# Optimization experiments

Measured on AMD Instinct MI355X. Metric: run time of the kernel, lower is better.

The kernel has to match this reference:

```python
import jax, jax.numpy as jnp
import numpy as np

B, C, H, W = 4, 512, 64, 64


def setup_inputs() -> dict:
    key = jax.random.key(0)
    k1, k2, k3, k4, k5 = jax.random.split(key, 5)
    s = 0.02
    return {
        "x": jax.random.normal(k1, (B, C, H, W), dtype=jnp.float32),
        "qkv_w": jax.random.normal(k2, (3 * C, C), dtype=jnp.float32) * s,
        "qkv_b": jax.random.normal(k3, (3 * C,), dtype=jnp.float32) * s,
        "proj_w": jax.random.normal(k4, (C, C), dtype=jnp.float32) * s,
        "proj_b": jax.random.normal(k5, (C,), dtype=jnp.float32) * s,
    }


def reference(x, qkv_w, qkv_b, proj_w, proj_b):
    # NOTE: the original module creates a GroupNorm but never calls it in
    # forward(), so x feeds the 1x1 qkv conv directly.
    b, c, h, w_ = x.shape
    n = h * w_
    xf = x.reshape(b, c, n)  # [B, C, N]
    # 1x1 conv == channel matmul
    qkv = jnp.einsum('oc,bcn->bon', qkv_w, xf) + qkv_b[None, :, None]  # [B, 3C, N]
    q, k, v = qkv[:, :c], qkv[:, c:2 * c], qkv[:, 2 * c:]
    scale = jnp.float32(c) ** -0.5
    # scores[b, i, j] = q_i . k_j  (i, j over spatial positions)
    scores = jnp.einsum('bci,bcj->bij', q, k) * scale  # [B, N, N]
    attn = jax.nn.softmax(scores, axis=2)
    # out_i = sum_j attn[i, j] * v_j
    hmat = jnp.einsum('bij,bcj->bci', attn, v)  # [B, C, N]
    out = jnp.einsum('oc,bcn->bon', proj_w, hmat) + proj_b[None, :, None]
    return x + out.reshape(b, c, h, w_)
```

## Files before the change

### kernel.cpp

```cpp
#include <hip/hip_runtime.h>


using u16 = unsigned short;
using u32 = unsigned int;
using h8   = __attribute__((ext_vector_type(8)))  short;
using fx4  = __attribute__((ext_vector_type(4)))  float;
using q16  = __attribute__((ext_vector_type(4)))  u32;
using u16x4= __attribute__((ext_vector_type(4)))  u16;

#define BB 4
#define CC 512
#define NN 4096
#define NBE ((size_t)BB * NN * CC)

#define GLOBAL_AS __attribute__((address_space(1)))
#define LDS_AS    __attribute__((address_space(3)))
#define GLOAD_LDS(src, dst) \
  __builtin_amdgcn_global_load_lds((const GLOBAL_AS u32*)(const void*)(src), \
                                   (LDS_AS u32*)(void*)(dst), 16, 0, 0)

__device__ __forceinline__ u16 f2b(float f) {
  u32 u = __float_as_uint(f);
  u = (u + 0x7fffu + ((u >> 16) & 1u)) >> 16;
  return (u16)u;
}
__device__ __forceinline__ float b2f(u16 h) { return __uint_as_float(((u32)h) << 16); }

__global__ void k_prep(const float* __restrict__ qw, const float* __restrict__ pw,
                       u16* __restrict__ wqb, u16* __restrict__ wpb) {
  int i = blockIdx.x * 256 + threadIdx.x;
  if (i < 1536 * 512) wqb[i] = f2b(qw[i]);
  if (i < 512 * 512)  wpb[i] = f2b(pw[i]);
}

__global__ __launch_bounds__(256) void k_txp(const float* __restrict__ x, u16* __restrict__ xt) {
  int bid = blockIdx.x;
  int nb = bid & 63; int cb = (bid >> 6) & 7; int b = bid >> 9;
  __shared__ float t[64][65];
  const float* xb = x + (size_t)b * CC * NN;
  for (int k = 0; k < 16; ++k) {
    int idx = k * 256 + threadIdx.x;
    int r = idx >> 6, col = idx & 63;
    t[r][col] = xb[(size_t)(cb * 64 + r) * NN + nb * 64 + col];
  }
  __syncthreads();
  u16* xtb = xt + (size_t)b * NN * CC;
  for (int k = 0; k < 16; ++k) {
    int idx = k * 256 + threadIdx.x;
    int nr = idx >> 6, cc = idx & 63;
    xtb[(size_t)(nb * 64 + nr) * CC + cb * 64 + cc] = f2b(t[cc][nr]);
  }
}

__device__ __forceinline__ void gemm_mm(const char* __restrict__ Ab, const char* __restrict__ Bb,
                                        q16* aT, q16* bT, fx4 (&acc)[4][4], int tid) {
  const int lane = tid & 63, wv = tid >> 6;
  const int wm = wv >> 1, wn = wv & 1, g = lane >> 4, r = lane & 15;
  for (int kb = 0; kb < 8; ++kb) {
    __syncthreads();
#pragma unroll
    for (int it = 0; it < 4; ++it) {
      int idx = it * 256 + tid; int row = idx >> 3, slot = idx & 7;
      size_t go = (size_t)row * 1024 + (size_t)kb * 128 + (size_t)slot * 16;
      aT[row * 8 + (slot ^ (row & 7))] = *(const q16*)(Ab + go);
      bT[row * 8 + (slot ^ (row & 7))] = *(const q16*)(Bb + go);
    }
    __syncthreads();
#pragma unroll
    for (int ks = 0; ks < 2; ++ks) {
      h8 af[4], bf[4];
#pragma unroll
      for (int mt = 0; mt < 4; ++mt) { int row = wm * 64 + mt * 16 + r; af[mt] = *(const h8*)&aT[row * 8 + ((ks * 4 + g) ^ (row & 7))]; }
#pragma unroll
      for (int nt = 0; nt < 4; ++nt) { int row = wn * 64 + nt * 16 + r; bf[nt] = *(const h8*)&bT[row * 8 + ((ks * 4 + g) ^ (row & 7))]; }
#pragma unroll
      for (int mt = 0; mt < 4; ++mt)
#pragma unroll
        for (int nt = 0; nt < 4; ++nt)
          acc[mt][nt] = __builtin_amdgcn_mfma_f32_16x16x32_bf16(af[mt], bf[nt], acc[mt][nt], 0, 0, 0);
    }
  }
}

__global__ __launch_bounds__(256) void k_qkv(const u16* __restrict__ wqb, const u16* __restrict__ xt,
                                             const float* __restrict__ qkvb,
                                             u16* __restrict__ qt, u16* __restrict__ kt, u16* __restrict__ vv) {
  __shared__ q16 aT[1024], bT[1024];
  int bid = blockIdx.x;
  int nb = bid & 31; int mb = (bid >> 5) % 12; int b = bid / 384;
  int ob = mb * 128, n0 = nb * 128;
  int tid = threadIdx.x, lane = tid & 63, wv = tid >> 6;
  int wm = wv >> 1, wn = wv & 1, g = lane >> 4, r = lane & 15;
  fx4 acc[4][4] = {};
  gemm_mm((const char*)(wqb + (size_t)ob * CC),
          (const char*)(xt + ((size_t)b * NN + n0) * CC), aT, bT, acc, tid);
  int region = mb >> 2;
#pragma unroll
  for (int mt = 0; mt < 4; ++mt) {
    int o_b = ob + wm * 64 + mt * 16 + g * 4;
#pragma unroll
    for (int nt = 0; nt < 4; ++nt) {
      int n = n0 + wn * 64 + nt * 16 + r;
      if (region == 2) {
#pragma unroll
        for (int rr = 0; rr < 4; ++rr) {
          int o = o_b + rr;
          float v = acc[mt][nt][rr] + qkvb[o];
          vv[((size_t)b * CC + (o - 1024)) * NN + n] = f2b(v);
        }
      } else {
        u16x4 pk;
#pragma unroll
        for (int rr = 0; rr < 4; ++rr) {
          int o = o_b + rr;
          float v = acc[mt][nt][rr] + qkvb[o];
          if (region == 0) v *= 0.044194173824159216f;
          pk[rr] = f2b(v);
        }
        u16* dst = (region == 0 ? qt : kt) + ((size_t)b * NN + n) * CC + (o_b - region * 512);
        *(u16x4*)dst = pk;
      }
    }
  }
}

#define BAR_VM() do { asm volatile("s_waitcnt vmcnt(0) lgkmcnt(0)" ::: "memory"); \
  __builtin_amdgcn_sched_barrier(0); __builtin_amdgcn_s_barrier(); \
  __builtin_amdgcn_sched_barrier(0); } while (0)

__global__ __launch_bounds__(512, 1) void k_attn(const u16* __restrict__ qt, const u16* __restrict__ kt,
                                                 const u16* __restrict__ vv,
                                                 u16* __restrict__ op, float* __restrict__ ml) {
  __shared__ __align__(16) q16 kbuf[2][2048];
  __shared__ __align__(16) q16 vbuf[2][2048];
  __shared__ __align__(16) u16 pT[8][16][40];

  int bid = blockIdx.x;
  int bp = bid & 7; int b = bp >> 1, part = bp & 1;
  int qb0 = (bid >> 3) * 128;
  int tid = threadIdx.x, w = tid >> 6, l = tid & 63;
  int g = l >> 4, r = l & 15;

  const u16* ktb = kt + (size_t)b * NN * CC;
  const u16* vvb = vv + (size_t)b * CC * NN;
  int j0 = part * 2048;

  h8 qf[16];
  {
    const u16* qrow = qt + ((size_t)b * NN + qb0 + w * 16 + r) * CC + g * 8;
#pragma unroll
    for (int ks = 0; ks < 16; ++ks) qf[ks] = *(const h8*)(qrow + ks * 32);
  }

  h8 ones;
#pragma unroll
  for (int e = 0; e < 8; ++e) ones[e] = (short)0x3F80;

  fx4 oacc[32] = {};
  fx4 lacc = {};

  const u16* ksrc0 = ktb + (size_t)w * CC + (size_t)((l ^ w) * 8);
  const int  vxr   = (l >> 3) & 3;
  const u16* vsrc0 = vvb + (size_t)(w * 16 + (l >> 2)) * NN + ((l & 3) ^ vxr) * 8;

#define STAGE(JB, D) do { \
  _Pragma("unroll") \
  for (int ro = 0; ro < 4; ++ro) { \
    int row = ro * 8 + w; \
    GLOAD_LDS(ksrc0 + ((size_t)(JB) + ro * 8) * CC, &kbuf[D][row * 64]); \
  } \
  _Pragma("unroll") \
  for (int ro = 0; ro < 4; ++ro) { \
    GLOAD_LDS(vsrc0 + (size_t)ro * 128 * NN + (JB), &vbuf[D][ro * 512 + w * 64]); \
  } \
} while (0)

  STAGE(j0, 0);
  BAR_VM();

  int cur = 0;
  for (int t = 0; t < 64; ++t) {
    if (t < 63) STAGE(j0 + t * 32 + 32, cur ^ 1);

    fx4 s[2] = {};
#pragma unroll
    for (int ks = 0; ks < 16; ++ks) {
#pragma unroll
      for (int nt = 0; nt < 2; ++nt) {
        int row = nt * 16 + r;
        h8 kf = *(const h8*)&kbuf[cur][row * 64 + ((ks * 4 + g) ^ (r & 7))];
        s[nt] = __builtin_amdgcn_mfma_f32_16x16x32_bf16(qf[ks], kf, s[nt], 0, 0, 0);
      }
    }

#pragma unroll
    for (int rr = 0; rr < 4; ++rr) {
      pT[w][g * 4 + rr][r]      = f2b(__expf(s[0][rr]));
      pT[w][g * 4 + rr][16 + r] = f2b(__expf(s[1][rr]));
    }
    asm volatile("s_waitcnt lgkmcnt(0)" ::: "memory");
    __builtin_amdgcn_sched_barrier(0);

    h8 pf = *(const h8*)&pT[w][r][g * 8];
    lacc = __builtin_amdgcn_mfma_f32_16x16x32_bf16(pf, ones, lacc, 0, 0, 0);
#pragma unroll
    for (int ct = 0; ct < 32; ++ct) {
      int c = ct * 16 + r;
      h8 vf = *(const h8*)&vbuf[cur][c * 4 + (g ^ ((r >> 1) & 3))];
      oacc[ct] = __builtin_amdgcn_mfma_f32_16x16x32_bf16(pf, vf, oacc[ct], 0, 0, 0);
    }

    BAR_VM();
    cur ^= 1;
  }

  u16* opb = op + (((size_t)part * BB + b) * NN + qb0 + w * 16) * CC;
#pragma unroll
  for (int ct = 0; ct < 32; ++ct)
#pragma unroll
    for (int rr = 0; rr < 4; ++rr) {
      int i = g * 4 + rr; int c = ct * 16 + r;
      opb[(size_t)i * CC + c] = f2b(oacc[ct][rr]);
    }
  if (r == 0) {
#pragma unroll
    for (int rr = 0; rr < 4; ++rr)
      ml[((size_t)part * BB + b) * NN + qb0 + w * 16 + g * 4 + rr] = lacc[rr];
  }
}

__global__ __launch_bounds__(256) void k_proj(const u16* __restrict__ op, const float* __restrict__ ml,
                                              const u16* __restrict__ wpb,
                                              const float* __restrict__ pb, const float* __restrict__ x,
                                              float* __restrict__ out) {
  __shared__ q16 aT[1024], bT[1024];
  __shared__ float invl[128];
  int bid = blockIdx.x;
  int ot = bid & 3; int ntile = (bid >> 2) & 31; int b = bid >> 7;
  int n0 = ntile * 128, o0 = ot * 128;
  int tid = threadIdx.x, lane = tid & 63, wv = tid >> 6;
  int wm = wv >> 1, wn = wv & 1, g = lane >> 4, r = lane & 15;

  if (tid < 128) {
    int n = n0 + tid;
    float l1 = ml[((size_t)0 * BB + b) * NN + n];
    float l2 = ml[((size_t)1 * BB + b) * NN + n];
    invl[tid] = 1.0f / (l1 + l2);
  }

  const char* Ab1 = (const char*)(op + ((size_t)b * NN + n0) * CC);
  const char* Ab2 = Ab1 + NBE * sizeof(u16);
  const char* Bb  = (const char*)(wpb + (size_t)o0 * CC);
  fx4 acc[4][4] = {};
  for (int kb = 0; kb < 8; ++kb) {
    __syncthreads();
#pragma unroll
    for (int it = 0; it < 4; ++it) {
      int idx = it * 256 + tid; int row = idx >> 3, slot = idx & 7;
      size_t go = (size_t)row * 1024 + (size_t)kb * 128 + (size_t)slot * 16;
      q16 a1 = *(const q16*)(Ab1 + go);
      q16 a2 = *(const q16*)(Ab2 + go);
      float iv = invl[row];
      u16 res[8];
      const u16* pa1 = (const u16*)&a1; const u16* pa2 = (const u16*)&a2;
#pragma unroll
      for (int e = 0; e < 8; ++e) res[e] = f2b((b2f(pa1[e]) + b2f(pa2[e])) * iv);
      aT[row * 8 + (slot ^ (row & 7))] = *(const q16*)res;
      bT[row * 8 + (slot ^ (row & 7))] = *(const q16*)(Bb + go);
    }
    __syncthreads();
#pragma unroll
    for (int ks = 0; ks < 2; ++ks) {
      h8 af[4], bf[4];
#pragma unroll
      for (int mt = 0; mt < 4; ++mt) { int row = wm * 64 + mt * 16 + r; af[mt] = *(const h8*)&aT[row * 8 + ((ks * 4 + g) ^ (row & 7))]; }
#pragma unroll
      for (int nt = 0; nt < 4; ++nt) { int row = wn * 64 + nt * 16 + r; bf[nt] = *(const h8*)&bT[row * 8 + ((ks * 4 + g) ^ (row & 7))]; }
#pragma unroll
      for (int mt = 0; mt < 4; ++mt)
#pragma unroll
        for (int nt = 0; nt < 4; ++nt)
          acc[mt][nt] = __builtin_amdgcn_mfma_f32_16x16x32_bf16(af[mt], bf[nt], acc[mt][nt], 0, 0, 0);
    }
  }
  const float* xb = x + (size_t)b * CC * NN;
  float* ob_ = out + (size_t)b * CC * NN;
#pragma unroll
  for (int nt = 0; nt < 4; ++nt) {
    int o = o0 + wn * 64 + nt * 16 + r;
    float bias = pb[o];
#pragma unroll
    for (int mt = 0; mt < 4; ++mt) {
      int n = n0 + wm * 64 + mt * 16 + g * 4;
      fx4 xv = *(const fx4*)(xb + (size_t)o * NN + n);
      fx4 res;
#pragma unroll
      for (int rr = 0; rr < 4; ++rr) res[rr] = acc[mt][nt][rr] + bias + xv[rr];
      *(fx4*)(ob_ + (size_t)o * NN + n) = res;
    }
  }
}

extern "C" void kernel_launch(void* const* d_in, const int* in_sizes, int n_in,
                              void* d_out, int out_size, void* d_ws, size_t ws_size,
                              hipStream_t stream) {
  const float* x  = (const float*)d_in[0];
  const float* qw = (const float*)d_in[1];
  const float* qb = (const float*)d_in[2];
  const float* pw = (const float*)d_in[3];
  const float* pb = (const float*)d_in[4];
  float* out = (float*)d_out;

  u16* ws  = (u16*)d_ws;
  u16* qt  = ws;
  u16* kt  = qt + NBE;
  u16* vv  = kt + NBE;
  u16* xt  = vv + NBE;
  u16* wqb = xt + NBE;
  u16* wpb = wqb + 1536 * 512;
  u16* op  = wpb + 512 * 512;
  float* ml = (float*)(op + 2 * NBE);

  hipLaunchKernelGGL(k_prep, dim3(3072), dim3(256), 0, stream, qw, pw, wqb, wpb);
  hipLaunchKernelGGL(k_txp,  dim3(2048), dim3(256), 0, stream, x, xt);
  hipLaunchKernelGGL(k_qkv,  dim3(1536), dim3(256), 0, stream, wqb, xt, qb, qt, kt, vv);
  hipLaunchKernelGGL(k_attn, dim3(256),  dim3(512), 0, stream, qt, kt, vv, op, ml);
  hipLaunchKernelGGL(k_proj, dim3(512),  dim3(256), 0, stream, op, ml, wpb, pb, x, out);
}
```

Measured before the change: 356.3 us.

## Switch attention Q/K/V and probabilities to FP8 MFMA

```diff
diff --git a/kernel.cpp b/kernel.cpp
--- a/kernel.cpp
+++ b/kernel.cpp
@@ -1,6 +1,7 @@
 #include <hip/hip_runtime.h>
 
 
+using u8  = unsigned char;
 using u16 = unsigned short;
 using u32 = unsigned int;
 using h8   = __attribute__((ext_vector_type(8)))  short;
@@ -12,6 +13,7 @@
 #define CC 512
 #define NN 4096
 #define NBE ((size_t)BB * NN * CC)
+#define SCALE 0.044194173824159216f
 
 #define GLOBAL_AS __attribute__((address_space(1)))
 #define LDS_AS    __attribute__((address_space(3)))
@@ -25,6 +27,9 @@
   return (u16)u;
 }
 __device__ __forceinline__ float b2f(u16 h) { return __uint_as_float(((u32)h) << 16); }
+__device__ __forceinline__ u8 f2f8(float f) {
+  return (u8)(u32)__builtin_amdgcn_cvt_pk_fp8_f32(f, 0.f, 0, false);
+}
 
 __global__ void k_prep(const float* __restrict__ qw, const float* __restrict__ pw,
                        u16* __restrict__ wqb, u16* __restrict__ wpb) {
@@ -84,7 +89,7 @@
 
 __global__ __launch_bounds__(256) void k_qkv(const u16* __restrict__ wqb, const u16* __restrict__ xt,
                                              const float* __restrict__ qkvb,
-                                             u16* __restrict__ qt, u16* __restrict__ kt, u16* __restrict__ vv) {
+                                             u8* __restrict__ qt, u8* __restrict__ kt, u8* __restrict__ vv) {
   __shared__ q16 aT[1024], bT[1024];
   int bid = blockIdx.x;
   int nb = bid & 31; int mb = (bid >> 5) % 12; int b = bid / 384;
@@ -101,24 +106,21 @@
 #pragma unroll
     for (int nt = 0; nt < 4; ++nt) {
       int n = n0 + wn * 64 + nt * 16 + r;
+      float v0 = acc[mt][nt][0] + qkvb[o_b + 0];
+      float v1 = acc[mt][nt][1] + qkvb[o_b + 1];
+      float v2 = acc[mt][nt][2] + qkvb[o_b + 2];
+      float v3 = acc[mt][nt][3] + qkvb[o_b + 3];
       if (region == 2) {
-#pragma unroll
-        for (int rr = 0; rr < 4; ++rr) {
-          int o = o_b + rr;
-          float v = acc[mt][nt][rr] + qkvb[o];
-          vv[((size_t)b * CC + (o - 1024)) * NN + n] = f2b(v);
-        }
+        u8* vb = vv + ((size_t)b * CC + (o_b - 1024)) * NN + n;
+        vb[0]          = f2f8(v0);
+        vb[NN]         = f2f8(v1);
+        vb[2 * NN]     = f2f8(v2);
+        vb[3 * (size_t)NN] = f2f8(v3);
       } else {
-        u16x4 pk;
-#pragma unroll
-        for (int rr = 0; rr < 4; ++rr) {
-          int o = o_b + rr;
-          float v = acc[mt][nt][rr] + qkvb[o];
-          if (region == 0) v *= 0.044194173824159216f;
-          pk[rr] = f2b(v);
-        }
-        u16* dst = (region == 0 ? qt : kt) + ((size_t)b * NN + n) * CC + (o_b - region * 512);
-        *(u16x4*)dst = pk;
+        int t = __builtin_amdgcn_cvt_pk_fp8_f32(v0, v1, 0, false);
+        t = __builtin_amdgcn_cvt_pk_fp8_f32(v2, v3, t, true);
+        u8* dst = (region == 0 ? qt : kt) + ((size_t)b * NN + n) * CC + (o_b - region * 512);
+        *(u32*)dst = (u32)t;
       }
     }
   }
@@ -128,12 +130,12 @@
   __builtin_amdgcn_sched_barrier(0); __builtin_amdgcn_s_barrier(); \
   __builtin_amdgcn_sched_barrier(0); } while (0)
 
-__global__ __launch_bounds__(512, 1) void k_attn(const u16* __restrict__ qt, const u16* __restrict__ kt,
-                                                 const u16* __restrict__ vv,
+__global__ __launch_bounds__(512, 1) void k_attn(const u8* __restrict__ qt, const u8* __restrict__ kt,
+                                                 const u8* __restrict__ vv,
                                                  u16* __restrict__ op, float* __restrict__ ml) {
-  __shared__ __align__(16) q16 kbuf[2][2048];
-  __shared__ __align__(16) q16 vbuf[2][2048];
-  __shared__ __align__(16) u16 pT[8][16][40];
+  __shared__ __align__(16) q16 kbuf[2][1024];
+  __shared__ __align__(16) q16 vbuf[2][1024];
+  __shared__ __align__(16) u8 pT[8][16][40];
 
   int bid = blockIdx.x;
   int bp = bid & 7; int b = bp >> 1, part = bp & 1;
@@ -141,38 +143,35 @@
   int tid = threadIdx.x, w = tid >> 6, l = tid & 63;
   int g = l >> 4, r = l & 15;
 
-  const u16* ktb = kt + (size_t)b * NN * CC;
-  const u16* vvb = vv + (size_t)b * CC * NN;
+  const u8* ktb = kt + (size_t)b * NN * CC;
+  const u8* vvb = vv + (size_t)b * CC * NN;
   int j0 = part * 2048;
 
-  h8 qf[16];
+  long qf[16];
   {
-    const u16* qrow = qt + ((size_t)b * NN + qb0 + w * 16 + r) * CC + g * 8;
-#pragma unroll
-    for (int ks = 0; ks < 16; ++ks) qf[ks] = *(const h8*)(qrow + ks * 32);
-  }
-
-  h8 ones;
-#pragma unroll
-  for (int e = 0; e < 8; ++e) ones[e] = (short)0x3F80;
+    const u8* qrow = qt + ((size_t)b * NN + qb0 + w * 16 + r) * CC + g * 8;
+#pragma unroll
+    for (int ks = 0; ks < 16; ++ks) qf[ks] = *(const long*)(qrow + ks * 32);
+  }
+
+  const long ones8 = 0x3838383838383838L;
 
   fx4 oacc[32] = {};
   fx4 lacc = {};
 
-  const u16* ksrc0 = ktb + (size_t)w * CC + (size_t)((l ^ w) * 8);
-  const int  vxr   = (l >> 3) & 3;
-  const u16* vsrc0 = vvb + (size_t)(w * 16 + (l >> 2)) * NN + ((l & 3) ^ vxr) * 8;
+  const int rk = w * 2 + (l >> 5);
+  const int ck = l & 31;
+  const size_t koff = (size_t)rk * CC + (size_t)((ck ^ (rk & 7)) * 16);
+  const int kdst = rk * 32 + ck;
+  const size_t voff = (size_t)(w * 32 + (l >> 1)) * NN + (l & 1) * 16;
+  const int vdst = (w * 32 + (l >> 1)) * 2 + (l & 1);
 
 #define STAGE(JB, D) do { \
-  _Pragma("unroll") \
-  for (int ro = 0; ro < 4; ++ro) { \
-    int row = ro * 8 + w; \
-    GLOAD_LDS(ksrc0 + ((size_t)(JB) + ro * 8) * CC, &kbuf[D][row * 64]); \
-  } \
-  _Pragma("unroll") \
-  for (int ro = 0; ro < 4; ++ro) { \
-    GLOAD_LDS(vsrc0 + (size_t)ro * 128 * NN + (JB), &vbuf[D][ro * 512 + w * 64]); \
-  } \
+  const u8* kb_ = ktb + (size_t)(JB) * CC; \
+  GLOAD_LDS(kb_ + koff,                  &kbuf[D][kdst]); \
+  GLOAD_LDS(kb_ + koff + (size_t)16*CC,  &kbuf[D][kdst + 512]); \
+  GLOAD_LDS(vvb + (JB) + voff,                     &vbuf[D][vdst]); \
+  GLOAD_LDS(vvb + (JB) + voff + (size_t)256 * NN,  &vbuf[D][vdst + 512]); \
 } while (0)
 
   STAGE(j0, 0);
@@ -183,31 +182,35 @@
     if (t < 63) STAGE(j0 + t * 32 + 32, cur ^ 1);
 
     fx4 s[2] = {};
+    const u8* kB = (const u8*)&kbuf[cur][0];
 #pragma unroll
     for (int ks = 0; ks < 16; ++ks) {
 #pragma unroll
       for (int nt = 0; nt < 2; ++nt) {
         int row = nt * 16 + r;
-        h8 kf = *(const h8*)&kbuf[cur][row * 64 + ((ks * 4 + g) ^ (r & 7))];
-        s[nt] = __builtin_amdgcn_mfma_f32_16x16x32_bf16(qf[ks], kf, s[nt], 0, 0, 0);
+        long kf = *(const long*)(kB + row * 512 + ((2 * ks + (g >> 1)) ^ (r & 7)) * 16 + (g & 1) * 8);
+        s[nt] = __builtin_amdgcn_mfma_f32_16x16x32_fp8_fp8(qf[ks], kf, s[nt], 0, 0, 0);
       }
     }
 
 #pragma unroll
     for (int rr = 0; rr < 4; ++rr) {
-      pT[w][g * 4 + rr][r]      = f2b(__expf(s[0][rr]));
-      pT[w][g * 4 + rr][16 + r] = f2b(__expf(s[1][rr]));
+      float p0 = __expf(s[0][rr] * SCALE);
+      float p1 = __expf(s[1][rr] * SCALE);
+      u32 pk = (u32)__builtin_amdgcn_cvt_pk_fp8_f32(p0, p1, 0, false);
+      pT[w][g * 4 + rr][r]      = (u8)pk;
+      pT[w][g * 4 + rr][16 + r] = (u8)(pk >> 8);
     }
     asm volatile("s_waitcnt lgkmcnt(0)" ::: "memory");
     __builtin_amdgcn_sched_barrier(0);
 
-    h8 pf = *(const h8*)&pT[w][r][g * 8];
-    lacc = __builtin_amdgcn_mfma_f32_16x16x32_bf16(pf, ones, lacc, 0, 0, 0);
+    long pf = *(const long*)&pT[w][r][g * 8];
+    lacc = __builtin_amdgcn_mfma_f32_16x16x32_fp8_fp8(pf, ones8, lacc, 0, 0, 0);
+    const u8* vB = (const u8*)&vbuf[cur][0];
 #pragma unroll
     for (int ct = 0; ct < 32; ++ct) {
-      int c = ct * 16 + r;
-      h8 vf = *(const h8*)&vbuf[cur][c * 4 + (g ^ ((r >> 1) & 3))];
-      oacc[ct] = __builtin_amdgcn_mfma_f32_16x16x32_bf16(pf, vf, oacc[ct], 0, 0, 0);
+      long vf = *(const long*)(vB + (ct * 16 + r) * 32 + g * 8);
+      oacc[ct] = __builtin_amdgcn_mfma_f32_16x16x32_fp8_fp8(pf, vf, oacc[ct], 0, 0, 0);
     }
 
     BAR_VM();
@@ -311,11 +314,11 @@
   const float* pb = (const float*)d_in[4];
   float* out = (float*)d_out;
 
-  u16* ws  = (u16*)d_ws;
-  u16* qt  = ws;
-  u16* kt  = qt + NBE;
-  u16* vv  = kt + NBE;
-  u16* xt  = vv + NBE;
+  u8* ws8 = (u8*)d_ws;
+  u8* qt  = ws8;
+  u8* kt  = qt + NBE;
+  u8* vv  = kt + NBE;
+  u16* xt  = (u16*)(vv + NBE);
   u16* wqb = xt + NBE;
   u16* wpb = wqb + 1536 * 512;
   u16* op  = wpb + 512 * 512;
```

After: 396.2 us. 1.11x slower.
